# Performance work log

Hardware: AMD Instinct MI355X
Metric: run time of the kernel (lower is better)

## Reference

```python
import jax, jax.numpy as jnp
import numpy as np

KERNEL_EPS = 1e-3   # generalized_kernel epsilon (performer)
Z_EPS = 1e-6        # LinearHopfieldCore eps


def _phi(x, proj):
    # generalized_kernel with relu: phi(x) = relu(d^{-0.25} * x @ P^T) + 1e-3
    # x: [B, L, H, D], proj: [M, D] -> [B, L, H, M]
    scale = x.shape[-1] ** -0.25
    return jax.nn.relu(jnp.einsum('blhd,md->blhm', x * scale, proj)) + KERNEL_EPS


def setup_inputs() -> dict:
    key = jax.random.key(0)
    kq, kk, kv, kp = jax.random.split(key, 4)
    B, L, H, D, M = 4, 4096, 16, 64, 256
    return {
        'q': jax.random.normal(kq, (B, L, H, D), dtype=jnp.float32),
        'k': jax.random.normal(kk, (B, L, H, D), dtype=jnp.float32),
        'v': jax.random.normal(kv, (B, L, H, D), dtype=jnp.float32),
        'projection_matrix': jax.random.normal(kp, (M, D), dtype=jnp.float32),
    }


def reference(q, k, v, projection_matrix):
    # Feature maps [B, L, H, M]
    Qf = _phi(q, projection_matrix)
    Kf = _phi(k, projection_matrix)
    # Linear attention (non-causal):
    # KV = sum_s K_s otimes V_s : [B, H, M, E]
    KV = jnp.einsum('bshm,bshe->bhme', Kf, v)
    # Z = 1 / (Q . (sum_s K_s + eps)) : [B, H, L]
    Ksum = jnp.sum(Kf, axis=1) + Z_EPS        # [B, H, M]
    Z = 1.0 / jnp.einsum('blhm,bhm->bhl', Qf, Ksum)
    # out = (Q @ KV) * Z : [B, L, H, E]
    out = jnp.einsum('bhme,blhm,bhl->blhe', KV, Qf, Z)
    return out
```

## Files before the change

kernel.cpp:

```cpp
#include <hip/hip_runtime.h>


#define LL 4096
#define HH 16
#define DD 64
#define EE 64
#define MM 256
#define SCALE 0.35355339059327378f

typedef __attribute__((ext_vector_type(8))) __bf16 bf8v;
typedef __attribute__((ext_vector_type(4))) __bf16 bf4v;
typedef __attribute__((ext_vector_type(4))) float f4v;

__device__ __forceinline__ __bf16 f2bf(float f) {
  union { float f; unsigned u; } x; x.f = f;
  unsigned r = (x.u + 0x7FFFu + ((x.u >> 16) & 1u)) >> 16;
  union { unsigned short s; __bf16 b; } y; y.s = (unsigned short)r;
  return y.b;
}

#define MFMA16(a, b, c) __builtin_amdgcn_mfma_f32_16x16x32_bf16(a, b, c, 0, 0, 0)

#define KV_ELEMS (64 * 64 * 256)
#define KSUM_OFF KV_ELEMS
#define WS_ZERO_BYTES ((size_t)(KV_ELEMS + 64 * 256) * 4)

__global__ __launch_bounds__(256, 2)
void k1_kv(const float* __restrict__ kin, const float* __restrict__ vin,
           const float* __restrict__ pin, float* __restrict__ ws) {
  __shared__ __bf16 kt[64 * 72];
  __shared__ __bf16 vt[64 * 68];
  __shared__ __bf16 kft[256 * 72];

  const int tid = threadIdx.x;
  const int wave = tid >> 6;
  const int lane = tid & 63;
  const int qd = lane >> 4;
  const int nn = lane & 15;
  const int bh = blockIdx.y;
  const int b = bh >> 4, h = bh & 15;
  const int l0 = blockIdx.x * 512;

  bf8v pf[4][2];
#pragma unroll
  for (int mt = 0; mt < 4; ++mt) {
    const float* pr = pin + (size_t)(64 * wave + mt * 16 + nn) * DD;
#pragma unroll
    for (int c = 0; c < 2; ++c) {
      bf8v t;
#pragma unroll
      for (int j = 0; j < 8; ++j) t[j] = f2bf(pr[c * 32 + qd * 8 + j] * SCALE);
      pf[mt][c] = t;
    }
  }

  f4v acc[4][4];
#pragma unroll
  for (int i = 0; i < 4; ++i)
#pragma unroll
    for (int j = 0; j < 4; ++j) acc[i][j] = (f4v){0.f, 0.f, 0.f, 0.f};
  float ksum[4] = {0.f, 0.f, 0.f, 0.f};

  const size_t bhbase = (size_t)b * LL * HH * DD + (size_t)h * DD;
  const int srow = tid >> 2;
  const int scol = (tid & 3) * 16;

  for (int it = 0; it < 8; ++it) {
    {
      const size_t g = bhbase + (size_t)(l0 + it * 64 + srow) * (HH * DD) + scol;
      const f4v* gk = (const f4v*)(kin + g);
      const f4v* gv = (const f4v*)(vin + g);
      f4v k0 = gk[0], k1 = gk[1], k2 = gk[2], k3 = gk[3];
      f4v v0 = gv[0], v1 = gv[1], v2 = gv[2], v3 = gv[3];
      bf8v w0, w1;
#pragma unroll
      for (int j = 0; j < 4; ++j) {
        w0[j] = f2bf(k0[j]); w0[j + 4] = f2bf(k1[j]);
        w1[j] = f2bf(k2[j]); w1[j + 4] = f2bf(k3[j]);
      }
      *(bf8v*)&kt[srow * 72 + scol] = w0;
      *(bf8v*)&kt[srow * 72 + scol + 8] = w1;
      bf4v x0, x1, x2, x3;
#pragma unroll
      for (int j = 0; j < 4; ++j) {
        x0[j] = f2bf(v0[j]); x1[j] = f2bf(v1[j]);
        x2[j] = f2bf(v2[j]); x3[j] = f2bf(v3[j]);
      }
      *(bf4v*)&vt[srow * 68 + scol] = x0;
      *(bf4v*)&vt[srow * 68 + scol + 4] = x1;
      *(bf4v*)&vt[srow * 68 + scol + 8] = x2;
      *(bf4v*)&vt[srow * 68 + scol + 12] = x3;
    }
    __syncthreads();

#pragma unroll
    for (int lt = 0; lt < 4; ++lt) {
      bf8v a0 = *(const bf8v*)&kt[(lt * 16 + nn) * 72 + qd * 8];
      bf8v a1 = *(const bf8v*)&kt[(lt * 16 + nn) * 72 + 32 + qd * 8];
#pragma unroll
      for (int mt = 0; mt < 4; ++mt) {
        f4v cc = (f4v){0.f, 0.f, 0.f, 0.f};
        cc = MFMA16(a0, pf[mt][0], cc);
        cc = MFMA16(a1, pf[mt][1], cc);
        bf4v pk;
#pragma unroll
        for (int r = 0; r < 4; ++r) {
          float ph = fmaxf(cc[r], 0.f) + 1e-3f;
          ksum[mt] += ph;
          pk[r] = f2bf(ph);
        }
        *(bf4v*)&kft[(64 * wave + mt * 16 + nn) * 72 + lt * 16 + qd * 4] = pk;
      }
    }

#pragma unroll
    for (int c = 0; c < 2; ++c) {
      bf8v af[4];
#pragma unroll
      for (int mt = 0; mt < 4; ++mt)
        af[mt] = *(const bf8v*)&kft[(64 * wave + mt * 16 + nn) * 72 + c * 32 + qd * 8];
#pragma unroll
      for (int et = 0; et < 4; ++et) {
        bf8v bv;
#pragma unroll
        for (int j = 0; j < 8; ++j) bv[j] = vt[(c * 32 + qd * 8 + j) * 68 + et * 16 + nn];
#pragma unroll
        for (int mt = 0; mt < 4; ++mt) acc[mt][et] = MFMA16(af[mt], bv, acc[mt][et]);
      }
    }
    __syncthreads();
  }

  float* kvb = ws + (size_t)bh * (64 * 256);
#pragma unroll
  for (int mt = 0; mt < 4; ++mt)
#pragma unroll
    for (int et = 0; et < 4; ++et) {
#pragma unroll
      for (int r = 0; r < 4; ++r) {
        int m = 64 * wave + mt * 16 + 4 * qd + r;
        int e = et * 16 + nn;
        atomicAdd(&kvb[e * 256 + m], acc[mt][et][r]);
      }
    }
#pragma unroll
  for (int mt = 0; mt < 4; ++mt) {
    float s = ksum[mt];
    s += __shfl_xor(s, 16, 64);
    s += __shfl_xor(s, 32, 64);
    if (lane < 16) atomicAdd(&ws[KSUM_OFF + bh * 256 + 64 * wave + mt * 16 + lane], s);
  }
}

__global__ __launch_bounds__(256, 2)
void k3_out(const float* __restrict__ qin, const float* __restrict__ pin,
            const float* __restrict__ ws, float* __restrict__ out) {
  __shared__ __bf16 qt[64 * 72];
  __shared__ __bf16 qf[64 * 264];
  __shared__ float denp[256];
  __shared__ float denr[64];
  __shared__ float ksume[256];

  const int tid = threadIdx.x;
  const int wave = tid >> 6;
  const int lane = tid & 63;
  const int qd = lane >> 4;
  const int nn = lane & 15;
  const int bh = blockIdx.y;
  const int b = bh >> 4, h = bh & 15;
  const int l0 = blockIdx.x * 512;

  bf8v pf[4][2];
#pragma unroll
  for (int mt = 0; mt < 4; ++mt) {
    const float* pr = pin + (size_t)(64 * wave + mt * 16 + nn) * DD;
#pragma unroll
    for (int c = 0; c < 2; ++c) {
      bf8v t;
#pragma unroll
      for (int j = 0; j < 8; ++j) t[j] = f2bf(pr[c * 32 + qd * 8 + j] * SCALE);
      pf[mt][c] = t;
    }
  }

  const float* kvb = ws + (size_t)bh * (64 * 256);
  bf8v kvf[8];
#pragma unroll
  for (int c = 0; c < 8; ++c) {
    const float* src = kvb + (size_t)(16 * wave + nn) * 256 + c * 32 + qd * 8;
    bf8v t;
#pragma unroll
    for (int j = 0; j < 8; ++j) t[j] = f2bf(src[j]);
    kvf[c] = t;
  }

  ksume[tid] = ws[KSUM_OFF + bh * 256 + tid] + 1e-6f;

  const size_t bhbase = (size_t)b * LL * HH * DD + (size_t)h * DD;
  const int srow = tid >> 2;
  const int scol = (tid & 3) * 16;

  for (int it = 0; it < 8; ++it) {
    {
      const f4v* gq = (const f4v*)(qin + bhbase + (size_t)(l0 + it * 64 + srow) * (HH * DD) + scol);
      f4v q0 = gq[0], q1 = gq[1], q2 = gq[2], q3 = gq[3];
      bf8v w0, w1;
#pragma unroll
      for (int j = 0; j < 4; ++j) {
        w0[j] = f2bf(q0[j]); w0[j + 4] = f2bf(q1[j]);
        w1[j] = f2bf(q2[j]); w1[j + 4] = f2bf(q3[j]);
      }
      *(bf8v*)&qt[srow * 72 + scol] = w0;
      *(bf8v*)&qt[srow * 72 + scol + 8] = w1;
    }
    __syncthreads();

#pragma unroll
    for (int lt = 0; lt < 4; ++lt) {
      bf8v b0 = *(const bf8v*)&qt[(lt * 16 + nn) * 72 + qd * 8];
      bf8v b1 = *(const bf8v*)&qt[(lt * 16 + nn) * 72 + 32 + qd * 8];
      float dpart = 0.f;
#pragma unroll
      for (int mt = 0; mt < 4; ++mt) {
        f4v cc = (f4v){0.f, 0.f, 0.f, 0.f};
        cc = MFMA16(pf[mt][0], b0, cc);
        cc = MFMA16(pf[mt][1], b1, cc);
        bf4v pk;
#pragma unroll
        for (int r = 0; r < 4; ++r) {
          float ph = fmaxf(cc[r], 0.f) + 1e-3f;
          dpart += ph * ksume[64 * wave + mt * 16 + 4 * qd + r];
          pk[r] = f2bf(ph);
        }
        *(bf4v*)&qf[(lt * 16 + nn) * 264 + 64 * wave + mt * 16 + 4 * qd] = pk;
      }
      dpart += __shfl_xor(dpart, 16, 64);
      dpart += __shfl_xor(dpart, 32, 64);
      if (lane < 16) denp[wave * 64 + lt * 16 + lane] = dpart;
    }
    __syncthreads();
    if (tid < 64)
      denr[tid] = 1.f / (denp[tid] + denp[64 + tid] + denp[128 + tid] + denp[192 + tid]);
    __syncthreads();

#pragma unroll
    for (int lt = 0; lt < 4; ++lt) {
      f4v co = (f4v){0.f, 0.f, 0.f, 0.f};
#pragma unroll
      for (int c = 0; c < 8; ++c) {
        bf8v af = *(const bf8v*)&qf[(lt * 16 + nn) * 264 + c * 32 + qd * 8];
        co = MFMA16(af, kvf[c], co);
      }
#pragma unroll
      for (int r = 0; r < 4; ++r) {
        int lrel = lt * 16 + 4 * qd + r;
        int labs = l0 + it * 64 + lrel;
        out[((size_t)((size_t)b * LL + labs) * HH + h) * EE + 16 * wave + nn] =
            co[r] * denr[lrel];
      }
    }
    __syncthreads();
  }
}

extern "C" void kernel_launch(void* const* d_in, const int* in_sizes, int n_in,
                              void* d_out, int out_size, void* d_ws, size_t ws_size,
                              hipStream_t stream) {
  (void)in_sizes; (void)n_in; (void)out_size;
  const float* q = (const float*)d_in[0];
  const float* k = (const float*)d_in[1];
  const float* v = (const float*)d_in[2];
  const float* p = (const float*)d_in[3];
  float* ws = (float*)d_ws;
  float* out = (float*)d_out;

  if (ws_size < WS_ZERO_BYTES) return;

  hipMemsetAsync(d_ws, 0, WS_ZERO_BYTES, stream);
  dim3 grid(8, 64), blk(256);
  k1_kv<<<grid, blk, 0, stream>>>(k, v, p, ws);
  k3_out<<<grid, blk, 0, stream>>>(q, p, ws, out);
}
```

Baseline: 335.4 us.

## Remove block barriers via per-wave LDS, direct K/Q loads, MFMA denominator

In the KV kernel each wave now loads K rows straight into MFMA registers and keeps its own private V and feature tiles in LDS, so the per-iteration block-wide barriers go away, although every wave now re-reads all of V. In the output kernel Q is loaded straight into registers, and the normalizer is computed as an extra MFMA against a bf16 Ksum vector. This replaces the shuffle/LDS reduction and two barriers, at the cost of bf16 precision in the denominator. The output grid is doubled with half the rows per block, and launch bounds are raised to 3 blocks per SM for more occupancy.

```diff
diff --git a/kernel.cpp b/kernel.cpp
--- a/kernel.cpp
+++ b/kernel.cpp
@@ -28,9 +28,8 @@
 __global__ __launch_bounds__(256, 2)
 void k1_kv(const float* __restrict__ kin, const float* __restrict__ vin,
            const float* __restrict__ pin, float* __restrict__ ws) {
-  __shared__ __bf16 kt[64 * 72];
-  __shared__ __bf16 vt[64 * 68];
-  __shared__ __bf16 kft[256 * 72];
+  __shared__ __bf16 vt[4 * 64 * 68];
+  __shared__ __bf16 kft[4 * 64 * 72];
 
   const int tid = threadIdx.x;
   const int wave = tid >> 6;
@@ -41,6 +40,9 @@
   const int b = bh >> 4, h = bh & 15;
   const int l0 = blockIdx.x * 512;
 
+  __bf16* vtw = vt + wave * (64 * 68);
+  __bf16* kftw = kft + wave * (64 * 72);
+
   bf8v pf[4][2];
 #pragma unroll
   for (int mt = 0; mt < 4; ++mt) {
@@ -62,41 +64,34 @@
   float ksum[4] = {0.f, 0.f, 0.f, 0.f};
 
   const size_t bhbase = (size_t)b * LL * HH * DD + (size_t)h * DD;
-  const int srow = tid >> 2;
-  const int scol = (tid & 3) * 16;
 
   for (int it = 0; it < 8; ++it) {
-    {
-      const size_t g = bhbase + (size_t)(l0 + it * 64 + srow) * (HH * DD) + scol;
-      const f4v* gk = (const f4v*)(kin + g);
-      const f4v* gv = (const f4v*)(vin + g);
-      f4v k0 = gk[0], k1 = gk[1], k2 = gk[2], k3 = gk[3];
-      f4v v0 = gv[0], v1 = gv[1], v2 = gv[2], v3 = gv[3];
-      bf8v w0, w1;
+    const int lt0 = l0 + it * 64;
+
+#pragma unroll
+    for (int t = 0; t < 16; ++t) {
+      int linear = t * 256 + lane * 4;
+      int row = linear >> 6, col = linear & 63;
+      f4v vv = *(const f4v*)(vin + bhbase + (size_t)(lt0 + row) * (HH * DD) + col);
+      bf4v x;
+#pragma unroll
+      for (int j = 0; j < 4; ++j) x[j] = f2bf(vv[j]);
+      *(bf4v*)&vtw[row * 68 + col] = x;
+    }
+
+#pragma unroll
+    for (int lt = 0; lt < 4; ++lt) {
+      const float* krow = kin + bhbase + (size_t)(lt0 + lt * 16 + nn) * (HH * DD) + qd * 8;
+      f4v ka0 = *(const f4v*)(krow);
+      f4v ka1 = *(const f4v*)(krow + 4);
+      f4v ka2 = *(const f4v*)(krow + 32);
+      f4v ka3 = *(const f4v*)(krow + 36);
+      bf8v a0, a1;
 #pragma unroll
       for (int j = 0; j < 4; ++j) {
-        w0[j] = f2bf(k0[j]); w0[j + 4] = f2bf(k1[j]);
-        w1[j] = f2bf(k2[j]); w1[j + 4] = f2bf(k3[j]);
-      }
-      *(bf8v*)&kt[srow * 72 + scol] = w0;
-      *(bf8v*)&kt[srow * 72 + scol + 8] = w1;
-      bf4v x0, x1, x2, x3;
-#pragma unroll
-      for (int j = 0; j < 4; ++j) {
-        x0[j] = f2bf(v0[j]); x1[j] = f2bf(v1[j]);
-        x2[j] = f2bf(v2[j]); x3[j] = f2bf(v3[j]);
-      }
-      *(bf4v*)&vt[srow * 68 + scol] = x0;
-      *(bf4v*)&vt[srow * 68 + scol + 4] = x1;
-      *(bf4v*)&vt[srow * 68 + scol + 8] = x2;
-      *(bf4v*)&vt[srow * 68 + scol + 12] = x3;
-    }
-    __syncthreads();
-
-#pragma unroll
-    for (int lt = 0; lt < 4; ++lt) {
-      bf8v a0 = *(const bf8v*)&kt[(lt * 16 + nn) * 72 + qd * 8];
-      bf8v a1 = *(const bf8v*)&kt[(lt * 16 + nn) * 72 + 32 + qd * 8];
+        a0[j] = f2bf(ka0[j]); a0[j + 4] = f2bf(ka1[j]);
+        a1[j] = f2bf(ka2[j]); a1[j + 4] = f2bf(ka3[j]);
+      }
 #pragma unroll
       for (int mt = 0; mt < 4; ++mt) {
         f4v cc = (f4v){0.f, 0.f, 0.f, 0.f};
@@ -109,7 +104,7 @@
           ksum[mt] += ph;
           pk[r] = f2bf(ph);
         }
-        *(bf4v*)&kft[(64 * wave + mt * 16 + nn) * 72 + lt * 16 + qd * 4] = pk;
+        *(bf4v*)&kftw[(mt * 16 + nn) * 72 + lt * 16 + qd * 4] = pk;
       }
     }
 
@@ -118,31 +113,29 @@
       bf8v af[4];
 #pragma unroll
       for (int mt = 0; mt < 4; ++mt)
-        af[mt] = *(const bf8v*)&kft[(64 * wave + mt * 16 + nn) * 72 + c * 32 + qd * 8];
+        af[mt] = *(const bf8v*)&kftw[(mt * 16 + nn) * 72 + c * 32 + qd * 8];
 #pragma unroll
       for (int et = 0; et < 4; ++et) {
         bf8v bv;
 #pragma unroll
-        for (int j = 0; j < 8; ++j) bv[j] = vt[(c * 32 + qd * 8 + j) * 68 + et * 16 + nn];
+        for (int j = 0; j < 8; ++j) bv[j] = vtw[(c * 32 + qd * 8 + j) * 68 + et * 16 + nn];
 #pragma unroll
         for (int mt = 0; mt < 4; ++mt) acc[mt][et] = MFMA16(af[mt], bv, acc[mt][et]);
       }
     }
-    __syncthreads();
   }
 
   float* kvb = ws + (size_t)bh * (64 * 256);
 #pragma unroll
   for (int mt = 0; mt < 4; ++mt)
 #pragma unroll
-    for (int et = 0; et < 4; ++et) {
+    for (int et = 0; et < 4; ++et)
 #pragma unroll
       for (int r = 0; r < 4; ++r) {
         int m = 64 * wave + mt * 16 + 4 * qd + r;
         int e = et * 16 + nn;
         atomicAdd(&kvb[e * 256 + m], acc[mt][et][r]);
       }
-    }
 #pragma unroll
   for (int mt = 0; mt < 4; ++mt) {
     float s = ksum[mt];
@@ -152,14 +145,10 @@
   }
 }
 
-__global__ __launch_bounds__(256, 2)
+__global__ __launch_bounds__(256, 3)
 void k3_out(const float* __restrict__ qin, const float* __restrict__ pin,
             const float* __restrict__ ws, float* __restrict__ out) {
-  __shared__ __bf16 qt[64 * 72];
   __shared__ __bf16 qf[64 * 264];
-  __shared__ float denp[256];
-  __shared__ float denr[64];
-  __shared__ float ksume[256];
 
   const int tid = threadIdx.x;
   const int wave = tid >> 6;
@@ -168,7 +157,7 @@
   const int nn = lane & 15;
   const int bh = blockIdx.y;
   const int b = bh >> 4, h = bh & 15;
-  const int l0 = blockIdx.x * 512;
+  const int l0 = blockIdx.x * 256;
 
   bf8v pf[4][2];
 #pragma unroll
@@ -193,33 +182,38 @@
     for (int j = 0; j < 8; ++j) t[j] = f2bf(src[j]);
     kvf[c] = t;
   }
-
-  ksume[tid] = ws[KSUM_OFF + bh * 256 + tid] + 1e-6f;
+  bf8v kvd[8];
+#pragma unroll
+  for (int c = 0; c < 8; ++c) {
+    const float* src = ws + KSUM_OFF + bh * 256 + c * 32 + qd * 8;
+    f4v s0 = *(const f4v*)src, s1 = *(const f4v*)(src + 4);
+    bf8v t;
+#pragma unroll
+    for (int j = 0; j < 4; ++j) {
+      t[j] = f2bf(s0[j] + 1e-6f);
+      t[j + 4] = f2bf(s1[j] + 1e-6f);
+    }
+    kvd[c] = t;
+  }
 
   const size_t bhbase = (size_t)b * LL * HH * DD + (size_t)h * DD;
-  const int srow = tid >> 2;
-  const int scol = (tid & 3) * 16;
-
-  for (int it = 0; it < 8; ++it) {
-    {
-      const f4v* gq = (const f4v*)(qin + bhbase + (size_t)(l0 + it * 64 + srow) * (HH * DD) + scol);
-      f4v q0 = gq[0], q1 = gq[1], q2 = gq[2], q3 = gq[3];
-      bf8v w0, w1;
+
+  for (int it = 0; it < 4; ++it) {
+    const int lt0 = l0 + it * 64;
+
+#pragma unroll
+    for (int lt = 0; lt < 4; ++lt) {
+      const float* qrow = qin + bhbase + (size_t)(lt0 + lt * 16 + nn) * (HH * DD) + qd * 8;
+      f4v qa0 = *(const f4v*)(qrow);
+      f4v qa1 = *(const f4v*)(qrow + 4);
+      f4v qa2 = *(const f4v*)(qrow + 32);
+      f4v qa3 = *(const f4v*)(qrow + 36);
+      bf8v b0, b1;
 #pragma unroll
       for (int j = 0; j < 4; ++j) {
-        w0[j] = f2bf(q0[j]); w0[j + 4] = f2bf(q1[j]);
-        w1[j] = f2bf(q2[j]); w1[j + 4] = f2bf(q3[j]);
-      }
-      *(bf8v*)&qt[srow * 72 + scol] = w0;
-      *(bf8v*)&qt[srow * 72 + scol + 8] = w1;
-    }
-    __syncthreads();
-
-#pragma unroll
-    for (int lt = 0; lt < 4; ++lt) {
-      bf8v b0 = *(const bf8v*)&qt[(lt * 16 + nn) * 72 + qd * 8];
-      bf8v b1 = *(const bf8v*)&qt[(lt * 16 + nn) * 72 + 32 + qd * 8];
-      float dpart = 0.f;
+        b0[j] = f2bf(qa0[j]); b0[j + 4] = f2bf(qa1[j]);
+        b1[j] = f2bf(qa2[j]); b1[j + 4] = f2bf(qa3[j]);
+      }
 #pragma unroll
       for (int mt = 0; mt < 4; ++mt) {
         f4v cc = (f4v){0.f, 0.f, 0.f, 0.f};
@@ -227,36 +221,28 @@
         cc = MFMA16(pf[mt][1], b1, cc);
         bf4v pk;
 #pragma unroll
-        for (int r = 0; r < 4; ++r) {
-          float ph = fmaxf(cc[r], 0.f) + 1e-3f;
-          dpart += ph * ksume[64 * wave + mt * 16 + 4 * qd + r];
-          pk[r] = f2bf(ph);
-        }
+        for (int r = 0; r < 4; ++r) pk[r] = f2bf(fmaxf(cc[r], 0.f) + 1e-3f);
         *(bf4v*)&qf[(lt * 16 + nn) * 264 + 64 * wave + mt * 16 + 4 * qd] = pk;
       }
-      dpart += __shfl_xor(dpart, 16, 64);
-      dpart += __shfl_xor(dpart, 32, 64);
-      if (lane < 16) denp[wave * 64 + lt * 16 + lane] = dpart;
-    }
-    __syncthreads();
-    if (tid < 64)
-      denr[tid] = 1.f / (denp[tid] + denp[64 + tid] + denp[128 + tid] + denp[192 + tid]);
+    }
     __syncthreads();
 
 #pragma unroll
     for (int lt = 0; lt < 4; ++lt) {
       f4v co = (f4v){0.f, 0.f, 0.f, 0.f};
+      f4v cd = (f4v){0.f, 0.f, 0.f, 0.f};
 #pragma unroll
       for (int c = 0; c < 8; ++c) {
         bf8v af = *(const bf8v*)&qf[(lt * 16 + nn) * 264 + c * 32 + qd * 8];
         co = MFMA16(af, kvf[c], co);
+        cd = MFMA16(af, kvd[c], cd);
       }
 #pragma unroll
       for (int r = 0; r < 4; ++r) {
         int lrel = lt * 16 + 4 * qd + r;
-        int labs = l0 + it * 64 + lrel;
+        int labs = lt0 + lrel;
         out[((size_t)((size_t)b * LL + labs) * HH + h) * EE + 16 * wave + nn] =
-            co[r] * denr[lrel];
+            co[r] / cd[r];
       }
     }
     __syncthreads();
@@ -277,7 +263,7 @@
   if (ws_size < WS_ZERO_BYTES) return;
 
   hipMemsetAsync(d_ws, 0, WS_ZERO_BYTES, stream);
-  dim3 grid(8, 64), blk(256);
-  k1_kv<<<grid, blk, 0, stream>>>(k, v, p, ws);
-  k3_out<<<grid, blk, 0, stream>>>(q, p, ws, out);
-}
+  dim3 blk(256);
+  k1_kv<<<dim3(8, 64), blk, 0, stream>>>(k, v, p, ws);
+  k3_out<<<dim3(16, 64), blk, 0, stream>>>(q, p, ws, out);
+}
```

Measured after the change: 439.2 us. +31.0%, slower.
